# Performance work log

Hardware: AMD Instinct MI355X
Metric: run time of the kernel (lower is better)

The kernel has to match this reference:

```python
import jax, jax.numpy as jnp
import numpy as np

DEPTH = 3  # chemprop default message passing depth


def setup_inputs() -> dict:
    key = jax.random.key(0)
    ks = jax.random.split(key, 10)
    n_atoms, n_bonds, max_nb, n_mols = 50000, 100000, 6, 2000
    atom_fdim, bond_fdim, hidden = 133, 147, 300
    f_atoms = jax.random.normal(ks[0], (n_atoms, atom_fdim), dtype=jnp.float32)
    f_bonds = jax.random.normal(ks[1], (n_bonds, bond_fdim), dtype=jnp.float32)
    a2b = jax.random.randint(ks[2], (n_atoms, max_nb), 0, n_bonds, dtype=jnp.int32)
    b2a = jax.random.randint(ks[3], (n_bonds,), 0, n_atoms, dtype=jnp.int32)
    b2revb = jax.random.randint(ks[4], (n_bonds,), 0, n_bonds, dtype=jnp.int32)
    mol_id = jnp.sort(jax.random.randint(ks[5], (n_atoms,), 0, n_mols, dtype=jnp.int32))
    W_i = jax.random.normal(ks[6], (bond_fdim, hidden), dtype=jnp.float32) * 0.05
    W_h = jax.random.normal(ks[7], (hidden, hidden), dtype=jnp.float32) * 0.05
    W_o = jax.random.normal(ks[8], (atom_fdim + hidden, hidden), dtype=jnp.float32) * 0.05
    b_o = jnp.zeros((hidden,), dtype=jnp.float32)
    return {"f_atoms": f_atoms, "f_bonds": f_bonds, "a2b": a2b, "b2a": b2a,
            "b2revb": b2revb, "mol_id": mol_id, "n_mols": n_mols,
            "W_i": W_i, "W_h": W_h, "W_o": W_o, "b_o": b_o}


def reference(f_atoms, f_bonds, a2b, b2a, b2revb, mol_id, n_mols, W_i, W_h, W_o, b_o):
    act = jax.nn.relu
    # W_i: bond features -> hidden; message init
    inp = f_bonds @ W_i                      # [n_bonds, h]
    message = act(inp)
    for _ in range(DEPTH - 1):
        nei = message[a2b]                    # [n_atoms, max_nb, h] gather
        a_message = nei.sum(axis=1)           # [n_atoms, h]
        rev = message[b2revb]                 # [n_bonds, h]
        message = a_message[b2a] - rev        # [n_bonds, h]
        message = act(inp + message @ W_h)
    # final atom readout
    a_message = message[a2b].sum(axis=1)      # [n_atoms, h]
    a_input = jnp.concatenate([f_atoms, a_message], axis=1)  # [n_atoms, fa+h]
    atom_hiddens = act(a_input @ W_o + b_o)   # [n_atoms, h]
    # ragged per-molecule mean (a_scope loop -> segment mean)
    sums = jax.ops.segment_sum(atom_hiddens, mol_id, num_segments=n_mols)
    counts = jax.ops.segment_sum(jnp.ones((atom_hiddens.shape[0],), dtype=atom_hiddens.dtype), mol_id, num_segments=n_mols)
    mol_vecs = jnp.where(counts[:, None] > 0, sums / jnp.maximum(counts, 1.0)[:, None], 0.0)
    return mol_vecs
```

## Files before the change

### kernel.cpp

```cpp
#include <hip/hip_runtime.h>
#include <cstddef>

#define H 300
#define RS 304
#define MAXNB 6
#define ASTR 312

typedef __attribute__((ext_vector_type(8)))  short bf16x8;
typedef __attribute__((ext_vector_type(16))) float f32x16;

__device__ __forceinline__ float bf2f(unsigned short u) {
    return __uint_as_float(((unsigned int)u) << 16);
}
__device__ __forceinline__ unsigned short f2bf(float f) {
    unsigned int u = __float_as_uint(f);
    u += 0x7FFFu + ((u >> 16) & 1u);
    return (unsigned short)(u >> 16);
}
__device__ __forceinline__ unsigned int sub2bf(unsigned int a, unsigned int b) {
    float d0 = bf2f((unsigned short)(a & 0xFFFFu)) - bf2f((unsigned short)(b & 0xFFFFu));
    float d1 = bf2f((unsigned short)(a >> 16))     - bf2f((unsigned short)(b >> 16));
    return (unsigned int)f2bf(d0) | ((unsigned int)f2bf(d1) << 16);
}
__device__ __forceinline__ unsigned int relu2(unsigned int w) {
    unsigned int r = w;
    if (w & 0x80000000u) r &= 0x0000FFFFu;
    if (w & 0x00008000u) r &= 0xFFFF0000u;
    return r;
}
__device__ __forceinline__ uint4 relu4(uint4 v) {
    v.x = relu2(v.x); v.y = relu2(v.y); v.z = relu2(v.z); v.w = relu2(v.w);
    return v;
}
__device__ __forceinline__ uint4 subpack4(uint4 a, uint4 b) {
    uint4 r;
    r.x = sub2bf(a.x, b.x); r.y = sub2bf(a.y, b.y);
    r.z = sub2bf(a.z, b.z); r.w = sub2bf(a.w, b.w);
    return r;
}


template<int S>
__global__ void __launch_bounds__(256)
pack_a_f32_c(const float* __restrict__ src, unsigned short* __restrict__ dst,
             int M, int K)
{
    __shared__ unsigned short sm[64 * 152];
    const int m0 = blockIdx.x * 64;
    const int r = threadIdx.x >> 2;
    const int q = threadIdx.x & 3;
    int mv = m0 + r; if (mv >= M) mv = M - 1;
    const float* rowF = src + (size_t)mv * K;
#pragma unroll
    for (int i = 0; i < (S * 4 + 3) / 4; ++i) {
        int c = q + i * 4;
        if (c * 4 < S * 16) {
            unsigned short h[4];
#pragma unroll
            for (int e = 0; e < 4; ++e) {
                int k = c * 4 + e;
                h[e] = (k < K) ? f2bf(rowF[k]) : (unsigned short)0;
            }
            uint2 o;
            o.x = (unsigned int)h[0] | ((unsigned int)h[1] << 16);
            o.y = (unsigned int)h[2] | ((unsigned int)h[3] << 16);
            *(uint2*)&sm[r * 152 + c * 4] = o;
        }
    }
    __syncthreads();
    for (int j = threadIdx.x; j < 2 * S * 64; j += 256) {
        int lane = j & 63;
        int t = j >> 6;
        int s = t % S;
        int mb2 = t / S;
        uint4 v = *(const uint4*)&sm[(mb2 * 32 + (lane & 31)) * 152 + s * 16 + (lane >> 5) * 8];
        int m_blk = blockIdx.x * 2 + mb2;
        *(uint4*)&dst[((size_t)(m_blk * S + s) * 64 + lane) * 8] = v;
    }
}

__global__ void __launch_bounds__(256)
pack_b(const float* __restrict__ src1, const float* __restrict__ src2,
       unsigned short* __restrict__ dst, int K1, int S1, int K2, int SB)
{
    int g = blockIdx.x * 256 + threadIdx.x;
    if (g >= 10 * SB * 64) return;
    int lane = g & 63;
    int t = g >> 6;
    int s = t % SB;
    int n_blk = t / SB;
    int n = n_blk * 32 + (lane & 31);
    unsigned int w[4];
#pragma unroll
    for (int p = 0; p < 4; ++p) {
        unsigned short h[2];
#pragma unroll
        for (int e = 0; e < 2; ++e) {
            int kf = s * 16 + (lane >> 5) * 8 + p * 2 + e;
            float v = 0.0f;
            if (n < H) {
                if (s < S1) {
                    if (kf < K1) v = src1[(size_t)kf * H + n];
                } else {
                    int k2 = kf - S1 * 16;
                    if (k2 < K2) v = src2[(size_t)k2 * H + n];
                }
            }
            h[e] = f2bf(v);
        }
        w[p] = (unsigned int)h[0] | ((unsigned int)h[1] << 16);
    }
    *(uint4*)&dst[(size_t)g * 8] = make_uint4(w[0], w[1], w[2], w[3]);
}

template<int RELU>
__global__ void __launch_bounds__(256)
aggregate_row(const unsigned short* __restrict__ msg, const int* __restrict__ a2b,
              unsigned short* __restrict__ amsg, int n_atoms)
{
    int gid = blockIdx.x * 256 + threadIdx.x;
    int total = n_atoms * 38;
    if (gid >= total) return;
    int atom = gid / 38;
    int g8 = gid - atom * 38;
    const int* nb = a2b + atom * MAXNB;
    float sum[8] = {};
#pragma unroll
    for (int j = 0; j < MAXNB; ++j) {
        int b = nb[j];
        uint4 v = *(const uint4*)&msg[(size_t)b * RS + g8 * 8];
        if (RELU) v = relu4(v);
        unsigned int ww[4] = {v.x, v.y, v.z, v.w};
#pragma unroll
        for (int p = 0; p < 4; ++p) {
            sum[p * 2]     += bf2f((unsigned short)(ww[p] & 0xFFFFu));
            sum[p * 2 + 1] += bf2f((unsigned short)(ww[p] >> 16));
        }
    }
    unsigned int ow[4];
#pragma unroll
    for (int p = 0; p < 4; ++p)
        ow[p] = (unsigned int)f2bf(sum[p * 2]) | ((unsigned int)f2bf(sum[p * 2 + 1]) << 16);
    *(uint4*)&amsg[(size_t)atom * RS + g8 * 8] = make_uint4(ow[0], ow[1], ow[2], ow[3]);
}

template<int S1, int S2, int SBL, int MODE, int RELUMSG>
__global__ void __launch_bounds__(640, 8)
gemm_fused(const unsigned short* __restrict__ A1,
           const unsigned short* __restrict__ amsg,
           const unsigned short* __restrict__ msg,
           const int* __restrict__ b2a, const int* __restrict__ b2revb,
           const unsigned short* __restrict__ Bp,
           const float* __restrict__ bias,
           const unsigned short* __restrict__ inp_add,
           const float* __restrict__ Adense, int Kd,
           unsigned short* __restrict__ out, int M)
{
    __shared__ __align__(16) unsigned short smem[64 * ASTR];

    const int lane  = threadIdx.x & 63;
    const int w     = threadIdx.x >> 6;
    const int mrow  = lane & 31;
    const int quad  = lane >> 5;
    const int m0    = blockIdx.x * 64;

    if (threadIdx.x < 512) {
        const int r = threadIdx.x >> 3;
        const int q = threadIdx.x & 7;
        int mm = m0 + r;
        int mv = (mm < M) ? mm : 0;
        if (MODE == 0) {
            if (mm >= M) mv = M - 1;
            const float* rowF = Adense + (size_t)mv * Kd;
#pragma unroll
            for (int i = 0; i < 5; ++i) {
                int c = q + i * 8;
                if (c * 4 < S2 * 16) {
                    unsigned short h[4];
#pragma unroll
                    for (int e = 0; e < 4; ++e) {
                        int k = c * 4 + e;
                        h[e] = (k < Kd) ? f2bf(rowF[k]) : (unsigned short)0;
                    }
                    uint2 o;
                    o.x = (unsigned int)h[0] | ((unsigned int)h[1] << 16);
                    o.y = (unsigned int)h[2] | ((unsigned int)h[3] << 16);
                    *(uint2*)&smem[r * ASTR + c * 4] = o;
                }
            }
        } else {
            const unsigned short* rowA;
            const unsigned short* rowM = nullptr;
            if (MODE == 1) {
                rowA = amsg + (size_t)b2a[mv] * RS;
                rowM = msg  + (size_t)b2revb[mv] * RS;
            } else {
                rowA = amsg + (size_t)mv * RS;
            }
#pragma unroll
            for (int i = 0; i < 5; ++i) {
                int c = q + i * 8;
                if (c < 38) {
                    uint4 o;
                    if (MODE == 1) {
                        uint4 va = *(const uint4*)(rowA + c * 8);
                        uint4 vm = *(const uint4*)(rowM + c * 8);
                        if (RELUMSG) vm = relu4(vm);
                        o = subpack4(va, vm);
                    } else {
                        o = *(const uint4*)(rowA + c * 8);
                    }
                    *(uint4*)&smem[r * ASTR + c * 8] = o;
                }
            }
        }
    }
    __syncthreads();

    f32x16 acc_lo, acc_hi;
#pragma unroll
    for (int i = 0; i < 16; ++i) { acc_lo[i] = 0.0f; acc_hi[i] = 0.0f; }

    const unsigned short* pa1_lo = (S1 > 0)
        ? (A1 + ((size_t)(blockIdx.x * 2 + 0) * S1 * 64 + lane) * 8) : nullptr;
    const unsigned short* pa1_hi = (S1 > 0)
        ? (A1 + ((size_t)(blockIdx.x * 2 + 1) * S1 * 64 + lane) * 8) : nullptr;
    const unsigned short* pb = Bp + ((size_t)w * SBL * 64 + lane) * 8;

    constexpr int STOT = S1 + S2;

    auto loadA = [&](int s, const unsigned short* pa1x, int half) -> bf16x8 {
        if (s < S1) return *(const bf16x8*)(pa1x + (size_t)s * 512);
        return *(const bf16x8*)&smem[((half << 5) + mrow) * ASTR + (s - S1) * 16 + quad * 8];
    };

    bf16x8 b0, b1;
    b0 = *(const bf16x8*)(pb);
    if (STOT > 1) b1 = *(const bf16x8*)(pb + 512);

#pragma unroll
    for (int s = 0; s < STOT; s += 2) {
        bf16x8 a_lo = loadA(s, pa1_lo, 0);
        bf16x8 a_hi = loadA(s, pa1_hi, 1);
        acc_lo = __builtin_amdgcn_mfma_f32_32x32x16_bf16(a_lo, b0, acc_lo, 0, 0, 0);
        acc_hi = __builtin_amdgcn_mfma_f32_32x32x16_bf16(a_hi, b0, acc_hi, 0, 0, 0);
        if (s + 2 < STOT) b0 = *(const bf16x8*)(pb + (size_t)(s + 2) * 512);
        if (s + 1 < STOT) {
            bf16x8 a_lo2 = loadA(s + 1, pa1_lo, 0);
            bf16x8 a_hi2 = loadA(s + 1, pa1_hi, 1);
            acc_lo = __builtin_amdgcn_mfma_f32_32x32x16_bf16(a_lo2, b1, acc_lo, 0, 0, 0);
            acc_hi = __builtin_amdgcn_mfma_f32_32x32x16_bf16(a_hi2, b1, acc_hi, 0, 0, 0);
            if (s + 3 < STOT) b1 = *(const bf16x8*)(pb + (size_t)(s + 3) * 512);
        }
    }

    __syncthreads();

    {
        int col = w * 32 + mrow;
        if (col < 308) {
#pragma unroll
            for (int r = 0; r < 16; ++r) {
                int row = (r & 3) + 8 * (r >> 2) + 4 * quad;
                smem[row * 308 + col] = f2bf(acc_lo[r]);
            }
#pragma unroll
            for (int r = 0; r < 16; ++r) {
                int row = 32 + (r & 3) + 8 * (r >> 2) + 4 * quad;
                smem[row * 308 + col] = f2bf(acc_hi[r]);
            }
        }
    }
    __syncthreads();

    for (int idx = threadIdx.x; idx < 64 * 76; idx += 640) {
        int row = idx / 76, gcol = idx - row * 76;
        int mm = m0 + row;
        if (mm >= M) continue;
        int c0 = gcol * 4;
        uint2 raw = *(const uint2*)&smem[row * 308 + c0];
        uint2 o;
        if (MODE == 0) {
            o = raw;
        } else {
            unsigned short h[4] = {(unsigned short)(raw.x & 0xFFFFu), (unsigned short)(raw.x >> 16),
                                   (unsigned short)(raw.y & 0xFFFFu), (unsigned short)(raw.y >> 16)};
            float v[4];
#pragma unroll
            for (int e = 0; e < 4; ++e) v[e] = bf2f(h[e]);
            if (MODE == 1) {
                uint2 iv = *(const uint2*)&inp_add[(size_t)mm * RS + c0];
                v[0] += bf2f((unsigned short)(iv.x & 0xFFFFu));
                v[1] += bf2f((unsigned short)(iv.x >> 16));
                v[2] += bf2f((unsigned short)(iv.y & 0xFFFFu));
                v[3] += bf2f((unsigned short)(iv.y >> 16));
            } else {
#pragma unroll
                for (int e = 0; e < 4; ++e) v[e] += (c0 + e < H) ? bias[c0 + e] : 0.0f;
            }
#pragma unroll
            for (int e = 0; e < 4; ++e) h[e] = f2bf(fmaxf(v[e], 0.0f));
            o.x = (unsigned int)h[0] | ((unsigned int)h[1] << 16);
            o.y = (unsigned int)h[2] | ((unsigned int)h[3] << 16);
        }
        *(uint2*)&out[(size_t)mm * RS + c0] = o;
    }
}

__global__ void __launch_bounds__(128)
segmean_kernel(const unsigned short* __restrict__ ah,
               const int* __restrict__ mol_id, int n_atoms,
               float* __restrict__ out)
{
    int m = blockIdx.x;
    int lo = 0, hi = n_atoms;
    while (lo < hi) { int mid = (lo + hi) >> 1; if (mol_id[mid] < m) lo = mid + 1; else hi = mid; }
    int start = lo;
    hi = n_atoms;
    while (lo < hi) { int mid = (lo + hi) >> 1; if (mol_id[mid] < m + 1) lo = mid + 1; else hi = mid; }
    int end = lo;

    int c = threadIdx.x;
    float a0 = 0.f, a1 = 0.f, a2 = 0.f;
    for (int a = start; a < end; ++a) {
        const unsigned short* row = ah + (size_t)a * RS;
        a0 += bf2f(row[c]);
        a1 += bf2f(row[c + 128]);
        if (c < H - 256) a2 += bf2f(row[c + 256]);
    }
    float inv = (end > start) ? 1.0f / (float)(end - start) : 0.0f;
    float* orow = out + (size_t)m * H;
    orow[c] = a0 * inv;
    orow[c + 128] = a1 * inv;
    if (c < H - 256) orow[c + 256] = a2 * inv;
}

extern "C" void kernel_launch(void* const* d_in, const int* in_sizes, int n_in,
                              void* d_out, int out_size, void* d_ws, size_t ws_size,
                              hipStream_t stream)
{
    const float* f_atoms = (const float*)d_in[0];
    const float* f_bonds = (const float*)d_in[1];
    const int*   a2b     = (const int*)d_in[2];
    const int*   b2a     = (const int*)d_in[3];
    const int*   b2revb  = (const int*)d_in[4];
    const int*   mol_id  = (const int*)d_in[5];
    const float* W_i     = (const float*)d_in[7];
    const float* W_h     = (const float*)d_in[8];
    const float* W_o     = (const float*)d_in[9];
    const float* b_o     = (const float*)d_in[10];

    const int n_atoms   = in_sizes[5];
    const int n_bonds   = in_sizes[3];
    const int atom_fdim = in_sizes[0] / n_atoms;
    const int bond_fdim = in_sizes[1] / n_bonds;
    const int n_mols    = out_size / H;

    const int gAtoms  = (n_atoms + 63) / 64;
    const int gBonds  = (n_bonds + 63) / 64;

    const size_t bondsRS = (size_t)n_bonds * RS;
    const size_t atomsRS = (size_t)n_atoms * RS;
    const size_t wihSz   = 10 * 30 * 512;
    const size_t woSz    = 10 * 29 * 512;
    const size_t wh19Sz  = 10 * 19 * 512;

    unsigned short* inp  = (unsigned short*)d_ws;
    unsigned short* msgB = inp  + bondsRS;
    unsigned short* amsg = msgB + bondsRS;
    unsigned short* wih  = amsg + atomsRS;
    unsigned short* wo   = wih  + wihSz;
    unsigned short* wh19 = wo   + woSz;
    unsigned short* ah   = wh19 + wh19Sz;
    unsigned short* fap  = inp;

    dim3 blk(256);
    dim3 gblk(640);
    const int aggBlocks = (n_atoms * 38 + 255) / 256;

    pack_b<<<(10 * 30 * 64 + 255) / 256, blk, 0, stream>>>(W_i, W_h, wih, bond_fdim, 10, H, 30);
    pack_b<<<(10 * 19 * 64 + 255) / 256, blk, 0, stream>>>(W_h, W_h, wh19, H, 19, 0, 19);
    pack_b<<<(10 * 29 * 64 + 255) / 256, blk, 0, stream>>>(W_o, W_o + (size_t)atom_fdim * H, wo,
                                                           atom_fdim, 9, H, 29);

    gemm_fused<0, 10, 30, 0, 0><<<gBonds, gblk, 0, stream>>>(
        nullptr, nullptr, nullptr, nullptr, nullptr, wih, nullptr, nullptr,
        f_bonds, bond_fdim, inp, n_bonds);

    aggregate_row<1><<<aggBlocks, blk, 0, stream>>>(inp, a2b, amsg, n_atoms);
    gemm_fused<0, 19, 19, 1, 1><<<gBonds, gblk, 0, stream>>>(
        nullptr, amsg, inp, b2a, b2revb, wh19, nullptr, inp, nullptr, 0, msgB, n_bonds);

    aggregate_row<0><<<aggBlocks, blk, 0, stream>>>(msgB, a2b, amsg, n_atoms);
    gemm_fused<0, 19, 19, 1, 0><<<gBonds, gblk, 0, stream>>>(
        nullptr, amsg, msgB, b2a, b2revb, wh19, nullptr, inp, nullptr, 0, inp, n_bonds);

    aggregate_row<0><<<aggBlocks, blk, 0, stream>>>(inp, a2b, amsg, n_atoms);

    pack_a_f32_c<9><<<gAtoms, blk, 0, stream>>>(f_atoms, fap, n_atoms, atom_fdim);

    gemm_fused<9, 19, 29, 2, 0><<<gAtoms, gblk, 0, stream>>>(
        fap, amsg, nullptr, nullptr, nullptr, wo, b_o, nullptr, nullptr, 0, ah, n_atoms);

    segmean_kernel<<<n_mols, dim3(128), 0, stream>>>(ah, mol_id, n_atoms, (float*)d_out);
}
```

Baseline: 482.8 us.

## Fuse final neighbor aggregation and atom-feature packing into readout GEMM

Adds a gemm_fused mode that builds the readout A tile in shared memory directly: it converts f_atoms rows to bf16 and gathers and sums the six neighbor messages per atom, instead of running a separate aggregate kernel and a pack kernel. This removes two launches and the global round trips through amsg and the packed f_atoms buffer. In exchange, shared memory per block grows to 456-element rows, which may lower occupancy, and the gather work now sits inside the GEMM prologue before the sync.

```diff
diff --git a/kernel.cpp b/kernel.cpp
--- a/kernel.cpp
+++ b/kernel.cpp
@@ -39,45 +39,6 @@
     return r;
 }
 
-
-template<int S>
-__global__ void __launch_bounds__(256)
-pack_a_f32_c(const float* __restrict__ src, unsigned short* __restrict__ dst,
-             int M, int K)
-{
-    __shared__ unsigned short sm[64 * 152];
-    const int m0 = blockIdx.x * 64;
-    const int r = threadIdx.x >> 2;
-    const int q = threadIdx.x & 3;
-    int mv = m0 + r; if (mv >= M) mv = M - 1;
-    const float* rowF = src + (size_t)mv * K;
-#pragma unroll
-    for (int i = 0; i < (S * 4 + 3) / 4; ++i) {
-        int c = q + i * 4;
-        if (c * 4 < S * 16) {
-            unsigned short h[4];
-#pragma unroll
-            for (int e = 0; e < 4; ++e) {
-                int k = c * 4 + e;
-                h[e] = (k < K) ? f2bf(rowF[k]) : (unsigned short)0;
-            }
-            uint2 o;
-            o.x = (unsigned int)h[0] | ((unsigned int)h[1] << 16);
-            o.y = (unsigned int)h[2] | ((unsigned int)h[3] << 16);
-            *(uint2*)&sm[r * 152 + c * 4] = o;
-        }
-    }
-    __syncthreads();
-    for (int j = threadIdx.x; j < 2 * S * 64; j += 256) {
-        int lane = j & 63;
-        int t = j >> 6;
-        int s = t % S;
-        int mb2 = t / S;
-        uint4 v = *(const uint4*)&sm[(mb2 * 32 + (lane & 31)) * 152 + s * 16 + (lane >> 5) * 8];
-        int m_blk = blockIdx.x * 2 + mb2;
-        *(uint4*)&dst[((size_t)(m_blk * S + s) * 64 + lane) * 8] = v;
-    }
-}
 
 __global__ void __launch_bounds__(256)
 pack_b(const float* __restrict__ src1, const float* __restrict__ src2,
@@ -156,7 +117,8 @@
            const float* __restrict__ Adense, int Kd,
            unsigned short* __restrict__ out, int M)
 {
-    __shared__ __align__(16) unsigned short smem[64 * ASTR];
+    constexpr int STR = (MODE == 3) ? 456 : 312;
+    __shared__ __align__(16) unsigned short smem[64 * STR];
 
     const int lane  = threadIdx.x & 63;
     const int w     = threadIdx.x >> 6;
@@ -185,7 +147,49 @@
                     uint2 o;
                     o.x = (unsigned int)h[0] | ((unsigned int)h[1] << 16);
                     o.y = (unsigned int)h[2] | ((unsigned int)h[3] << 16);
-                    *(uint2*)&smem[r * ASTR + c * 4] = o;
+                    *(uint2*)&smem[r * STR + c * 4] = o;
+                }
+            }
+        } else if (MODE == 3) {
+            const float* rowF = Adense + (size_t)mv * Kd;
+            const int* nb = b2a + mv * MAXNB;
+#pragma unroll
+            for (int i = 0; i < 7; ++i) {
+                int c = q + i * 8;
+                if (c < 18) {
+                    unsigned short h[8];
+#pragma unroll
+                    for (int e = 0; e < 8; ++e) {
+                        int k = c * 8 + e;
+                        h[e] = (k < Kd) ? f2bf(rowF[k]) : (unsigned short)0;
+                    }
+                    uint4 o;
+                    o.x = (unsigned int)h[0] | ((unsigned int)h[1] << 16);
+                    o.y = (unsigned int)h[2] | ((unsigned int)h[3] << 16);
+                    o.z = (unsigned int)h[4] | ((unsigned int)h[5] << 16);
+                    o.w = (unsigned int)h[6] | ((unsigned int)h[7] << 16);
+                    *(uint4*)&smem[r * STR + c * 8] = o;
+                } else if (c < 56) {
+                    int cc = c - 18;
+                    float sum[8] = {};
+#pragma unroll
+                    for (int j = 0; j < MAXNB; ++j) {
+                        uint4 v = *(const uint4*)&msg[(size_t)nb[j] * RS + cc * 8];
+                        unsigned int ww[4] = {v.x, v.y, v.z, v.w};
+#pragma unroll
+                        for (int p = 0; p < 4; ++p) {
+                            sum[p * 2]     += bf2f((unsigned short)(ww[p] & 0xFFFFu));
+                            sum[p * 2 + 1] += bf2f((unsigned short)(ww[p] >> 16));
+                        }
+                    }
+                    uint4 o;
+                    unsigned int ow[4];
+#pragma unroll
+                    for (int p = 0; p < 4; ++p)
+                        ow[p] = (unsigned int)f2bf(sum[p * 2]) |
+                                ((unsigned int)f2bf(sum[p * 2 + 1]) << 16);
+                    o = make_uint4(ow[0], ow[1], ow[2], ow[3]);
+                    *(uint4*)&smem[r * STR + 144 + cc * 8] = o;
                 }
             }
         } else {
@@ -210,7 +214,7 @@
                     } else {
                         o = *(const uint4*)(rowA + c * 8);
                     }
-                    *(uint4*)&smem[r * ASTR + c * 8] = o;
+                    *(uint4*)&smem[r * STR + c * 8] = o;
                 }
             }
         }
@@ -221,17 +225,19 @@
 #pragma unroll
     for (int i = 0; i < 16; ++i) { acc_lo[i] = 0.0f; acc_hi[i] = 0.0f; }
 
-    const unsigned short* pa1_lo = (S1 > 0)
+    const unsigned short* pa1_lo = (MODE != 3 && S1 > 0)
         ? (A1 + ((size_t)(blockIdx.x * 2 + 0) * S1 * 64 + lane) * 8) : nullptr;
-    const unsigned short* pa1_hi = (S1 > 0)
+    const unsigned short* pa1_hi = (MODE != 3 && S1 > 0)
         ? (A1 + ((size_t)(blockIdx.x * 2 + 1) * S1 * 64 + lane) * 8) : nullptr;
     const unsigned short* pb = Bp + ((size_t)w * SBL * 64 + lane) * 8;
 
     constexpr int STOT = S1 + S2;
 
     auto loadA = [&](int s, const unsigned short* pa1x, int half) -> bf16x8 {
-        if (s < S1) return *(const bf16x8*)(pa1x + (size_t)s * 512);
-        return *(const bf16x8*)&smem[((half << 5) + mrow) * ASTR + (s - S1) * 16 + quad * 8];
+        if (MODE != 3 && S1 > 0 && s < S1)
+            return *(const bf16x8*)(pa1x + (size_t)s * 512);
+        int off = (MODE == 3) ? s * 16 : (s - S1) * 16;
+        return *(const bf16x8*)&smem[((half << 5) + mrow) * STR + off + quad * 8];
     };
 
     bf16x8 b0, b1;
@@ -372,7 +378,6 @@
     unsigned short* wo   = wih  + wihSz;
     unsigned short* wh19 = wo   + woSz;
     unsigned short* ah   = wh19 + wh19Sz;
-    unsigned short* fap  = inp;
 
     dim3 blk(256);
     dim3 gblk(640);
@@ -395,12 +400,9 @@
     gemm_fused<0, 19, 19, 1, 0><<<gBonds, gblk, 0, stream>>>(
         nullptr, amsg, msgB, b2a, b2revb, wh19, nullptr, inp, nullptr, 0, inp, n_bonds);
 
-    aggregate_row<0><<<aggBlocks, blk, 0, stream>>>(inp, a2b, amsg, n_atoms);
-
-    pack_a_f32_c<9><<<gAtoms, blk, 0, stream>>>(f_atoms, fap, n_atoms, atom_fdim);
-
-    gemm_fused<9, 19, 29, 2, 0><<<gAtoms, gblk, 0, stream>>>(
-        fap, amsg, nullptr, nullptr, nullptr, wo, b_o, nullptr, nullptr, 0, ah, n_atoms);
+    gemm_fused<9, 19, 29, 3, 0><<<gAtoms, gblk, 0, stream>>>(
+        nullptr, nullptr, inp, a2b, nullptr, wo, b_o, nullptr,
+        f_atoms, atom_fdim, ah, n_atoms);
 
     segmean_kernel<<<n_mols, dim3(128), 0, stream>>>(ah, mol_id, n_atoms, (float*)d_out);
 }
```

Measured after the change: 475.2 us. Within noise of the previous version (-1.6%).

## Fuse final neighbor aggregation into readout GEMM and merge weight-pack launches

Applied to the files above, without the earlier changes.

Adds a MODE 3 path to the fused GEMM that gathers and sums the six neighbor bond messages per atom straight into shared memory. This removes the last aggregate_row launch and the write and re-read of the amsg buffer. The three weight-packing kernels are also merged into one launch, and the packed f_atoms buffer moves to msgB so it does not overwrite the final messages held in inp. The cost is heavier gather work inside the GEMM prologue, which may lengthen the staging phase before the MFMA loop.

```diff
diff --git a/kernel.cpp b/kernel.cpp
--- a/kernel.cpp
+++ b/kernel.cpp
@@ -79,11 +79,10 @@
     }
 }
 
-__global__ void __launch_bounds__(256)
-pack_b(const float* __restrict__ src1, const float* __restrict__ src2,
-       unsigned short* __restrict__ dst, int K1, int S1, int K2, int SB)
-{
-    int g = blockIdx.x * 256 + threadIdx.x;
+__device__ __forceinline__ void
+pack_b_body(int g, const float* __restrict__ src1, const float* __restrict__ src2,
+            unsigned short* __restrict__ dst, int K1, int S1, int K2, int SB)
+{
     if (g >= 10 * SB * 64) return;
     int lane = g & 63;
     int t = g >> 6;
@@ -111,6 +110,25 @@
         w[p] = (unsigned int)h[0] | ((unsigned int)h[1] << 16);
     }
     *(uint4*)&dst[(size_t)g * 8] = make_uint4(w[0], w[1], w[2], w[3]);
+}
+
+__global__ void __launch_bounds__(256)
+pack_b_all(const float* __restrict__ Wi, const float* __restrict__ Wh,
+           const float* __restrict__ Wo,
+           unsigned short* __restrict__ wih, unsigned short* __restrict__ wh19,
+           unsigned short* __restrict__ wo, int bond_fdim, int atom_fdim)
+{
+    const int B0 = (10 * 30 * 64 + 255) / 256;
+    const int B1 = (10 * 19 * 64 + 255) / 256;
+    int b = blockIdx.x;
+    if (b < B0) {
+        pack_b_body(b * 256 + threadIdx.x, Wi, Wh, wih, bond_fdim, 10, H, 30);
+    } else if (b < B0 + B1) {
+        pack_b_body((b - B0) * 256 + threadIdx.x, Wh, Wh, wh19, H, 19, 0, 19);
+    } else {
+        pack_b_body((b - B0 - B1) * 256 + threadIdx.x, Wo,
+                    Wo + (size_t)atom_fdim * H, wo, atom_fdim, 9, H, 29);
+    }
 }
 
 template<int RELU>
@@ -186,6 +204,31 @@
                     o.x = (unsigned int)h[0] | ((unsigned int)h[1] << 16);
                     o.y = (unsigned int)h[2] | ((unsigned int)h[3] << 16);
                     *(uint2*)&smem[r * ASTR + c * 4] = o;
+                }
+            }
+        } else if (MODE == 3) {
+            const int* nb = b2a + mv * MAXNB;
+#pragma unroll
+            for (int i = 0; i < 5; ++i) {
+                int c = q + i * 8;
+                if (c < 38) {
+                    float sum[8] = {};
+#pragma unroll
+                    for (int j = 0; j < MAXNB; ++j) {
+                        uint4 v = *(const uint4*)&msg[(size_t)nb[j] * RS + c * 8];
+                        unsigned int ww[4] = {v.x, v.y, v.z, v.w};
+#pragma unroll
+                        for (int p = 0; p < 4; ++p) {
+                            sum[p * 2]     += bf2f((unsigned short)(ww[p] & 0xFFFFu));
+                            sum[p * 2 + 1] += bf2f((unsigned short)(ww[p] >> 16));
+                        }
+                    }
+                    unsigned int ow[4];
+#pragma unroll
+                    for (int p = 0; p < 4; ++p)
+                        ow[p] = (unsigned int)f2bf(sum[p * 2]) |
+                                ((unsigned int)f2bf(sum[p * 2 + 1]) << 16);
+                    *(uint4*)&smem[r * ASTR + c * 8] = make_uint4(ow[0], ow[1], ow[2], ow[3]);
                 }
             }
         } else {
@@ -230,7 +273,7 @@
     constexpr int STOT = S1 + S2;
 
     auto loadA = [&](int s, const unsigned short* pa1x, int half) -> bf16x8 {
-        if (s < S1) return *(const bf16x8*)(pa1x + (size_t)s * 512);
+        if (S1 > 0 && s < S1) return *(const bf16x8*)(pa1x + (size_t)s * 512);
         return *(const bf16x8*)&smem[((half << 5) + mrow) * ASTR + (s - S1) * 16 + quad * 8];
     };
 
@@ -372,16 +415,16 @@
     unsigned short* wo   = wih  + wihSz;
     unsigned short* wh19 = wo   + woSz;
     unsigned short* ah   = wh19 + wh19Sz;
-    unsigned short* fap  = inp;
+    unsigned short* fap  = msgB;
 
     dim3 blk(256);
     dim3 gblk(640);
     const int aggBlocks = (n_atoms * 38 + 255) / 256;
-
-    pack_b<<<(10 * 30 * 64 + 255) / 256, blk, 0, stream>>>(W_i, W_h, wih, bond_fdim, 10, H, 30);
-    pack_b<<<(10 * 19 * 64 + 255) / 256, blk, 0, stream>>>(W_h, W_h, wh19, H, 19, 0, 19);
-    pack_b<<<(10 * 29 * 64 + 255) / 256, blk, 0, stream>>>(W_o, W_o + (size_t)atom_fdim * H, wo,
-                                                           atom_fdim, 9, H, 29);
+    const int packBlocks = (10 * 30 * 64 + 255) / 256 + (10 * 19 * 64 + 255) / 256
+                         + (10 * 29 * 64 + 255) / 256;
+
+    pack_b_all<<<packBlocks, blk, 0, stream>>>(W_i, W_h, W_o, wih, wh19, wo,
+                                               bond_fdim, atom_fdim);
 
     gemm_fused<0, 10, 30, 0, 0><<<gBonds, gblk, 0, stream>>>(
         nullptr, nullptr, nullptr, nullptr, nullptr, wih, nullptr, nullptr,
@@ -395,12 +438,11 @@
     gemm_fused<0, 19, 19, 1, 0><<<gBonds, gblk, 0, stream>>>(
         nullptr, amsg, msgB, b2a, b2revb, wh19, nullptr, inp, nullptr, 0, inp, n_bonds);
 
-    aggregate_row<0><<<aggBlocks, blk, 0, stream>>>(inp, a2b, amsg, n_atoms);
-
     pack_a_f32_c<9><<<gAtoms, blk, 0, stream>>>(f_atoms, fap, n_atoms, atom_fdim);
 
-    gemm_fused<9, 19, 29, 2, 0><<<gAtoms, gblk, 0, stream>>>(
-        fap, amsg, nullptr, nullptr, nullptr, wo, b_o, nullptr, nullptr, 0, ah, n_atoms);
+    gemm_fused<9, 19, 29, 3, 0><<<gAtoms, gblk, 0, stream>>>(
+        fap, nullptr, inp, a2b, nullptr, wo, b_o, nullptr,
+        nullptr, 0, ah, n_atoms);
 
     segmean_kernel<<<n_mols, dim3(128), 0, stream>>>(ah, mol_id, n_atoms, (float*)d_out);
 }
```

Result: no change. 473.6 us (-1.9%).
